# Performance work log

Measured on AMD Instinct MI355X. Metric: run time of the kernel, lower is better.

The kernel has to match this reference:

```python
import jax, jax.numpy as jnp
import numpy as np

N_NODES = 100000
N_GRAPHS = 64


def gcn_layer(x, src, dst, W, b, n):
    # GCNConv: h = x @ W; out_i = sum_j norm_ij * h_j (+ self loop), + bias
    h = x @ W
    deg = jax.ops.segment_sum(jnp.ones(src.shape[0], x.dtype), dst, num_segments=n)
    dinv = jnp.where(deg > 0, jax.lax.rsqrt(deg), 0.0)
    norm = dinv[src] * dinv[dst]                      # [E+N]
    agg = jax.ops.segment_sum(h[src] * norm[:, None], dst, num_segments=n)
    return agg + b


def setup_inputs() -> dict:
    key = jax.random.key(0)
    ks = jax.random.split(key, 12)
    nfeat, nhid, nclass = 128, 64, 10
    E = 1600000
    x = jax.random.normal(ks[0], (N_NODES, nfeat), dtype=jnp.float32)
    edge_index = jax.random.randint(ks[1], (2, E), 0, N_NODES, dtype=jnp.int64)
    batch = jnp.sort(jax.random.randint(ks[2], (N_NODES,), 0, N_GRAPHS, dtype=jnp.int64))
    def w(k, fi, fo):
        return jax.random.normal(k, (fi, fo), dtype=jnp.float32) / np.sqrt(fi)
    return {
        "x": x, "edge_index": edge_index, "batch": batch,
        "W1": w(ks[3], nfeat, nhid), "b1": jnp.zeros((nhid,), jnp.float32),
        "W2": w(ks[4], nhid, nhid), "b2": jnp.zeros((nhid,), jnp.float32),
        "W3": w(ks[5], nhid, nhid), "b3": jnp.zeros((nhid,), jnp.float32),
        "Wl": w(ks[6], nhid, nclass), "bl": jnp.zeros((nclass,), jnp.float32),
    }


def reference(x, edge_index, batch, W1, b1, W2, b2, W3, b3, Wl, bl):
    n = x.shape[0]
    loop = jnp.arange(n, dtype=edge_index.dtype)
    src = jnp.concatenate([edge_index[0], loop])   # self-loops appended
    dst = jnp.concatenate([edge_index[1], loop])
    h = x  # eval mode: dropout is identity; use_bn=False
    for W, b in ((W1, b1), (W2, b2), (W3, b3)):
        h = jax.nn.relu(gcn_layer(h, src, dst, W, b, n))
    # global mean pool per graph
    sums = jax.ops.segment_sum(h, batch, num_segments=N_GRAPHS)
    cnts = jax.ops.segment_sum(jnp.ones((n,), h.dtype), batch, num_segments=N_GRAPHS)
    pooled = sums / jnp.maximum(cnts, 1.0)[:, None]   # [G, nhid]
    logits = pooled @ Wl + bl
    return jax.nn.softmax(logits, axis=1)
```

## Files before the change

kernel.cpp:

```cpp
#include <hip/hip_runtime.h>
#include <math.h>


typedef __attribute__((ext_vector_type(8))) short bf16x8;
typedef __attribute__((ext_vector_type(4))) float f32x4;
typedef __attribute__((ext_vector_type(2))) float f32x2;

__device__ __forceinline__ unsigned short f2bf(float f) {
    unsigned int u = __float_as_uint(f);
    u += 0x7fffu + ((u >> 16) & 1u);
    return (unsigned short)(u >> 16);
}
__device__ __forceinline__ float bf2f(unsigned short u) {
    return __uint_as_float((unsigned int)u << 16);
}
__device__ __forceinline__ float bflo(unsigned int u) {
    return __uint_as_float(u << 16);
}
__device__ __forceinline__ float bfhi(unsigned int u) {
    return __uint_as_float(u & 0xffff0000u);
}


__global__ __launch_bounds__(256) void hist_kernel(const int* __restrict__ dst,
                                                   int* __restrict__ counts,
                                                   int E, int P, int C,
                                                   const float* __restrict__ W1,
                                                   const float* __restrict__ W2,
                                                   const float* __restrict__ W3,
                                                   unsigned short* __restrict__ Wt1,
                                                   unsigned short* __restrict__ Wt2,
                                                   unsigned short* __restrict__ Wt3,
                                                   float* __restrict__ sums, int G) {
    int t = threadIdx.x, b = blockIdx.x;
    if (b >= 256) {
        int xb = b - 256;
        if (xb < 3) {
            const float* W = (xb == 0) ? W1 : ((xb == 1) ? W2 : W3);
            unsigned short* Wt = (xb == 0) ? Wt1 : ((xb == 1) ? Wt2 : Wt3);
            int K = (xb == 0) ? 128 : 64;
            int o = t & 63;
            for (int k = t >> 6; k < K; k += 4)
                Wt[o * K + k] = f2bf(W[k * 64 + o]);
        } else {
            for (int i = t; i < G * 65; i += 256) sums[i] = 0.f;
        }
        return;
    }
    __shared__ int hist[256];
    if (t < P) hist[t] = 0;
    __syncthreads();
    int beg = b * C, end = min(E, beg + C);
    for (int base = beg + t * 8; base < end; base += 2048) {
        if (base + 8 <= end) {
            int4 d0 = *(const int4*)&dst[base];
            int4 d1 = *(const int4*)&dst[base + 4];
            int d[8] = {d0.x, d0.y, d0.z, d0.w, d1.x, d1.y, d1.z, d1.w};
#pragma unroll
            for (int j = 0; j < 8; ++j) atomicAdd(&hist[d[j] >> 9], 1);
        } else {
            for (int e = base; e < end; ++e) atomicAdd(&hist[dst[e] >> 9], 1);
        }
    }
    __syncthreads();
    if (t < P) counts[b * 256 + t] = hist[t];
}

__global__ __launch_bounds__(256) void pscan_kernel(const int* __restrict__ counts,
                                                    int* __restrict__ pbase,
                                                    int P) {
    __shared__ int s[256];
    int t = threadIdx.x;
    int v = 0;
    if (t < P)
        for (int b = 0; b < 256; ++b) v += counts[b * 256 + t];
    s[t] = v;
    __syncthreads();
    for (int off = 1; off < 256; off <<= 1) {
        int u = (t >= off) ? s[t - off] : 0;
        __syncthreads();
        s[t] += u;
        __syncthreads();
    }
    if (t < P) pbase[t] = s[t] - v;
    if (t == 255) pbase[P] = s[255];
}

__global__ __launch_bounds__(256) void offs_kernel(const int* __restrict__ counts,
                                                   const int* __restrict__ pbase,
                                                   int* __restrict__ offs) {
    __shared__ int s[256];
    int t = threadIdx.x, p = blockIdx.x;
    int v = counts[t * 256 + p];
    s[t] = v;
    __syncthreads();
    for (int off = 1; off < 256; off <<= 1) {
        int u = (t >= off) ? s[t - off] : 0;
        __syncthreads();
        s[t] += u;
        __syncthreads();
    }
    offs[p * 256 + t] = pbase[p] + s[t] - v;
}

__global__ __launch_bounds__(256) void bin_kernel(const int* __restrict__ src,
                                                  const int* __restrict__ dst,
                                                  const int* __restrict__ offs,
                                                  unsigned int* __restrict__ binned,
                                                  int E, int P, int C) {
    __shared__ int cur[256];
    int t = threadIdx.x, b = blockIdx.x;
    if (t < P) cur[t] = offs[t * 256 + b];
    __syncthreads();
    int beg = b * C, end = min(E, beg + C);
    for (int base = beg + t * 8; base < end; base += 2048) {
        if (base + 8 <= end) {
            int4 d0 = *(const int4*)&dst[base];
            int4 d1 = *(const int4*)&dst[base + 4];
            int4 s0 = *(const int4*)&src[base];
            int4 s1 = *(const int4*)&src[base + 4];
            int d[8] = {d0.x, d0.y, d0.z, d0.w, d1.x, d1.y, d1.z, d1.w};
            int s[8] = {s0.x, s0.y, s0.z, s0.w, s1.x, s1.y, s1.z, s1.w};
#pragma unroll
            for (int j = 0; j < 8; ++j) {
                int pos = atomicAdd(&cur[d[j] >> 9], 1);
                binned[pos] = ((unsigned int)s[j] << 9) | (unsigned int)(d[j] & 511);
            }
        } else {
            for (int e = base; e < end; ++e) {
                int dd = dst[e], ss = src[e];
                int pos = atomicAdd(&cur[dd >> 9], 1);
                binned[pos] = ((unsigned int)ss << 9) | (unsigned int)(dd & 511);
            }
        }
    }
}

__global__ __launch_bounds__(256) void gemm1_kernel(const float* __restrict__ X,
                                                    const unsigned short* __restrict__ Wt,
                                                    unsigned short* __restrict__ H, int N) {
    constexpr int FIN = 128;
    constexpr int KS = FIN / 32;
    constexpr int LDP = FIN + 8;
    __shared__ unsigned short sX[64 * LDP];
    int t = threadIdx.x;
    int rowBase = blockIdx.x * 64;

    for (int i = t * 4; i < 64 * FIN; i += 1024) {
        int r = i / FIN, c = i - r * FIN;
        int gr = min(rowBase + r, N - 1);
        float4 vv = *(const float4*)(X + (size_t)gr * FIN + c);
        unsigned e0 = __float_as_uint(vv.x) + 0x8000u, e1 = __float_as_uint(vv.y) + 0x8000u;
        unsigned e2 = __float_as_uint(vv.z) + 0x8000u, e3 = __float_as_uint(vv.w) + 0x8000u;
        uint2 pk;
        pk.x = __builtin_amdgcn_perm(e1, e0, 0x07060302);
        pk.y = __builtin_amdgcn_perm(e3, e2, 0x07060302);
        *(uint2*)&sX[r * LDP + c] = pk;
    }
    __syncthreads();

    int wave = t >> 6;
    int lane = t & 63;
    int r = lane & 15, g = lane >> 4;
    int node = rowBase + wave * 16 + r;

    bf16x8 afr[4][KS];
#pragma unroll
    for (int m = 0; m < 4; ++m)
#pragma unroll
        for (int s = 0; s < KS; ++s)
            afr[m][s] = *(const bf16x8*)&Wt[(m * 16 + r) * FIN + s * 32 + g * 8];

    f32x4 acc[4];
#pragma unroll
    for (int m = 0; m < 4; ++m) acc[m] = (f32x4){0.f, 0.f, 0.f, 0.f};

#pragma unroll
    for (int s = 0; s < KS; ++s) {
        bf16x8 bfr = *(const bf16x8*)&sX[(wave * 16 + r) * LDP + s * 32 + g * 8];
#pragma unroll
        for (int m = 0; m < 4; ++m)
            acc[m] = __builtin_amdgcn_mfma_f32_16x16x32_bf16(afr[m][s], bfr, acc[m], 0, 0, 0);
    }

    if (node < N) {
#pragma unroll
        for (int m = 0; m < 4; ++m) {
            ushort4 o;
            o.x = f2bf(acc[m][0]); o.y = f2bf(acc[m][1]);
            o.z = f2bf(acc[m][2]); o.w = f2bf(acc[m][3]);
            *(ushort4*)&H[(size_t)node * 64 + m * 16 + g * 4] = o;
        }
    }
}

__global__ __launch_bounds__(512) void lsort_kernel(const unsigned int* __restrict__ binned,
                                                    const int* __restrict__ pbase,
                                                    float* __restrict__ dinv,
                                                    int* __restrict__ ovfw,
                                                    int* __restrict__ csrw,
                                                    int* __restrict__ ovf, int N) {
    __shared__ int ldeg[512];
    __shared__ int s[512];
    __shared__ int sob[512];
    int t = threadIdx.x, p = blockIdx.x;
    int lo = p << 9;
    ldeg[t] = 0;
    __syncthreads();
    int eBeg = pbase[p], eEnd = pbase[p + 1];
    {
        int j = eBeg + t;
        for (; j + 1536 < eEnd; j += 2048) {
            unsigned int v0 = binned[j], v1 = binned[j + 512];
            unsigned int v2 = binned[j + 1024], v3 = binned[j + 1536];
            atomicAdd(&ldeg[v0 & 511u], 1);
            atomicAdd(&ldeg[v1 & 511u], 1);
            atomicAdd(&ldeg[v2 & 511u], 1);
            atomicAdd(&ldeg[v3 & 511u], 1);
        }
        for (; j < eEnd; j += 512) atomicAdd(&ldeg[binned[j] & 511u], 1);
    }
    __syncthreads();
    int real = ldeg[t];
    int deg1 = real + 1;
    int ovfUsed = (lo + t < N) ? max(deg1 - 24, 0) : 0;
    int gsl = ((ovfUsed + 7) >> 3) << 3;
    s[t] = gsl;
    __syncthreads();
    for (int off = 1; off < 512; off <<= 1) {
        int u = (t >= off) ? s[t - off] : 0;
        __syncthreads();
        s[t] += u;
        __syncthreads();
    }
    int obase = ((eBeg + 7) & ~7) + (p << 12);
    int myOvf = obase + (s[t] - gsl);
    int ow = gsl ? (((myOvf >> 3) << 7) | (gsl >> 3)) : 0;
    if (lo + t < N) {
        dinv[lo + t] = rsqrtf((float)deg1);
        ovfw[lo + t] = ow;
    }
    if (p == 0 && t == 0) dinv[N] = 0.f;
    __syncthreads();
    ldeg[t] = 0;
    sob[t] = myOvf;
    __syncthreads();
    {
        int j = eBeg + t;
        for (; j + 1536 < eEnd; j += 2048) {
            unsigned int v[4] = {binned[j], binned[j + 512],
                                 binned[j + 1024], binned[j + 1536]};
#pragma unroll
            for (int q = 0; q < 4; ++q) {
                int sr = (int)(v[q] >> 9);
                int dl = (int)(v[q] & 511u);
                int i = atomicAdd(&ldeg[dl], 1);
                int ent = sr << 7;
                if (i < 24) csrw[(size_t)(lo + dl) * 24 + i] = ent;
                else        ovf[sob[dl] + i - 24] = ent;
            }
        }
        for (; j < eEnd; j += 512) {
            unsigned int vv = binned[j];
            int sr = (int)(vv >> 9);
            int dl = (int)(vv & 511u);
            int i = atomicAdd(&ldeg[dl], 1);
            int ent = sr << 7;
            if (i < 24) csrw[(size_t)(lo + dl) * 24 + i] = ent;
            else        ovf[sob[dl] + i - 24] = ent;
        }
    }
    __syncthreads();
    if (lo + t < N) {
        int node = lo + t;
        int dcur = ldeg[t];
        int self = node << 7;
        if (dcur < 24) csrw[(size_t)node * 24 + dcur] = self;
        else           ovf[sob[t] + dcur - 24] = self;
        int pad = N << 7;
        for (int k = dcur + 1; k < 24; ++k)
            csrw[(size_t)node * 24 + k] = pad;
        int og = (ow & 127) << 3;
        for (int k = max(dcur + 1 - 24, 0); k < og; ++k)
            ovf[sob[t] + k] = pad;
    }
}

template <int FIN>
__global__ __launch_bounds__(256) void gemm_mfma_kernel(const unsigned short* __restrict__ Xv,
                                                        const unsigned short* __restrict__ Wt,
                                                        unsigned short* __restrict__ H,
                                                        int N) {
    constexpr int KS = FIN / 32;
    constexpr int LDP = FIN + 8;
    __shared__ unsigned short sX[64 * LDP];
    int tid = threadIdx.x;
    int rowBase = blockIdx.x * 64;

    for (int i = tid * 8; i < 64 * FIN; i += 2048) {
        int r = i / FIN, c = i - r * FIN;
        int gr = min(rowBase + r, N - 1);
        uint4 vv = *(const uint4*)(Xv + (size_t)gr * FIN + c);
        *(uint4*)&sX[r * LDP + c] = vv;
    }
    __syncthreads();

    int wave = tid >> 6;
    int lane = tid & 63;
    int r = lane & 15, g = lane >> 4;
    int node = rowBase + wave * 16 + r;

    bf16x8 afr[4][KS];
#pragma unroll
    for (int m = 0; m < 4; ++m)
#pragma unroll
        for (int s = 0; s < KS; ++s)
            afr[m][s] = *(const bf16x8*)&Wt[(m * 16 + r) * FIN + s * 32 + g * 8];

    f32x4 acc[4];
#pragma unroll
    for (int m = 0; m < 4; ++m) acc[m] = (f32x4){0.f, 0.f, 0.f, 0.f};

#pragma unroll
    for (int s = 0; s < KS; ++s) {
        bf16x8 bfr = *(const bf16x8*)&sX[(wave * 16 + r) * LDP + s * 32 + g * 8];
#pragma unroll
        for (int m = 0; m < 4; ++m)
            acc[m] = __builtin_amdgcn_mfma_f32_16x16x32_bf16(afr[m][s], bfr, acc[m], 0, 0, 0);
    }

    if (node < N) {
#pragma unroll
        for (int m = 0; m < 4; ++m) {
            ushort4 o;
            o.x = f2bf(acc[m][0]); o.y = f2bf(acc[m][1]);
            o.z = f2bf(acc[m][2]); o.w = f2bf(acc[m][3]);
            *(ushort4*)&H[(size_t)node * 64 + m * 16 + g * 4] = o;
        }
    }
}

template <int NQ>
__device__ __forceinline__ void gstep(const int* __restrict__ csrw,
                                      const float* __restrict__ dinv,
                                      const char* __restrict__ hb, float di,
                                      int e, int g, int fo, f32x2 acc[4]) {
    int c[NQ];
#pragma unroll
    for (int q = 0; q < NQ; ++q) c[q] = csrw[e + 8 * q + g];
    float w[NQ];
    uint4 u[NQ];
#pragma unroll
    for (int q = 0; q < NQ; ++q) w[q] = dinv[c[q] >> 7];
#pragma unroll
    for (int q = 0; q < NQ; ++q)
        u[q] = *(const uint4*)(hb + c[q] + fo);
#pragma unroll
    for (int q = 0; q < NQ; ++q) {
        float wq = w[q] * di;
        f32x2 w2;
        w2.x = wq; w2.y = wq;
        acc[0] = __builtin_elementwise_fma(w2, (f32x2){bflo(u[q].x), bfhi(u[q].x)}, acc[0]);
        acc[1] = __builtin_elementwise_fma(w2, (f32x2){bflo(u[q].y), bfhi(u[q].y)}, acc[1]);
        acc[2] = __builtin_elementwise_fma(w2, (f32x2){bflo(u[q].z), bfhi(u[q].z)}, acc[2]);
        acc[3] = __builtin_elementwise_fma(w2, (f32x2){bflo(u[q].w), bfhi(u[q].w)}, acc[3]);
    }
}

__global__ __launch_bounds__(256) void gather_kernel(const int* __restrict__ csrw,
                                                     const int* __restrict__ ovf,
                                                     const int* __restrict__ ovfw,
                                                     const float* __restrict__ dinv,
                                                     const unsigned short* __restrict__ h,
                                                     const float* __restrict__ b,
                                                     unsigned short* __restrict__ aggb, int N) {
    int node = (blockIdx.x * 256 + threadIdx.x) >> 6;
    int lane = threadIdx.x & 63;
    if (node >= N) return;
    int g = lane >> 3;
    int f = lane & 7;
    int fo = f * 16;
    float di = dinv[node];

    f32x2 acc[4];
#pragma unroll
    for (int k = 0; k < 4; ++k) acc[k] = (f32x2){0.f, 0.f};

    const char* hb = (const char*)h;
    gstep<3>(csrw, dinv, hb, di, node * 24, g, fo, acc);

    int ow = ovfw[node];
    if (ow) {
        int onb = ow & 127;
        int oe = (ow >> 7) << 3;
        while (onb >= 4) { gstep<4>(ovf, dinv, hb, di, oe, g, fo, acc); oe += 32; onb -= 4; }
        if (onb == 3)      gstep<3>(ovf, dinv, hb, di, oe, g, fo, acc);
        else if (onb == 2) gstep<2>(ovf, dinv, hb, di, oe, g, fo, acc);
        else if (onb == 1) gstep<1>(ovf, dinv, hb, di, oe, g, fo, acc);
    }

    float a[8];
#pragma unroll
    for (int k = 0; k < 4; ++k) { a[2 * k] = acc[k].x; a[2 * k + 1] = acc[k].y; }
#pragma unroll
    for (int k = 0; k < 8; ++k) {
        float v = a[k];
        v += __shfl_xor(v, 8);
        v += __shfl_xor(v, 16);
        v += __shfl_xor(v, 32);
        a[k] = v;
    }
    if (g == 0) {
        float4 bv0 = *(const float4*)&b[f * 8];
        float4 bv1 = *(const float4*)&b[f * 8 + 4];
        float a0 = fmaxf(a[0] + bv0.x, 0.f), a1 = fmaxf(a[1] + bv0.y, 0.f);
        float a2 = fmaxf(a[2] + bv0.z, 0.f), a3 = fmaxf(a[3] + bv0.w, 0.f);
        float a4 = fmaxf(a[4] + bv1.x, 0.f), a5 = fmaxf(a[5] + bv1.y, 0.f);
        float a6 = fmaxf(a[6] + bv1.z, 0.f), a7 = fmaxf(a[7] + bv1.w, 0.f);
        uint4 o;
        o.x = ((unsigned)f2bf(a1) << 16) | f2bf(a0);
        o.y = ((unsigned)f2bf(a3) << 16) | f2bf(a2);
        o.z = ((unsigned)f2bf(a5) << 16) | f2bf(a4);
        o.w = ((unsigned)f2bf(a7) << 16) | f2bf(a6);
        *(uint4*)&aggb[((size_t)node << 6) + f * 8] = o;
    }
}

__global__ __launch_bounds__(256) void pool_kernel(const unsigned short* __restrict__ hb,
                                                   const int* __restrict__ batch,
                                                   float* __restrict__ sums,
                                                   float* __restrict__ cnts, int N) {
    int lane = threadIdx.x & 63;
    int wid = (blockIdx.x * 256 + threadIdx.x) >> 6;
    int base = wid * 32;
    if (base >= N) return;
    int nn = min(N - base, 32);
    int bl = batch[base + min(lane & 31, nn - 1)];

    float v[32];
#pragma unroll
    for (int j = 0; j < 32; ++j) {
        int node = base + min(j, nn - 1);
        v[j] = bf2f(hb[(size_t)node * 64 + lane]);
    }

    int curg = __shfl(bl, 0);
    float acc = 0.f, cnt = 0.f;
#pragma unroll
    for (int j = 0; j < 32; ++j) {
        if (j < nn) {
            int g = __shfl(bl, j);
            if (g != curg) {
                atomicAdd(&sums[curg * 64 + lane], acc);
                if (lane == 0) atomicAdd(&cnts[curg], cnt);
                acc = 0.f; cnt = 0.f; curg = g;
            }
            acc += v[j]; cnt += 1.f;
        }
    }
    atomicAdd(&sums[curg * 64 + lane], acc);
    if (lane == 0) atomicAdd(&cnts[curg], cnt);
}

__global__ void final_kernel(const float* __restrict__ sums, const float* __restrict__ cnts,
                             const float* __restrict__ Wl, const float* __restrict__ bl,
                             float* __restrict__ out, int G) {
    int g = blockIdx.x * blockDim.x + threadIdx.x;
    if (g >= G) return;
    float inv = 1.0f / fmaxf(cnts[g], 1.0f);
    float logits[10];
#pragma unroll
    for (int k = 0; k < 10; ++k) logits[k] = bl[k];
    for (int c = 0; c < 64; ++c) {
        float p = sums[g * 64 + c] * inv;
#pragma unroll
        for (int k = 0; k < 10; ++k) logits[k] = fmaf(p, Wl[c * 10 + k], logits[k]);
    }
    float m = logits[0];
#pragma unroll
    for (int k = 1; k < 10; ++k) m = fmaxf(m, logits[k]);
    float se = 0.f;
#pragma unroll
    for (int k = 0; k < 10; ++k) { logits[k] = expf(logits[k] - m); se += logits[k]; }
    float is = 1.0f / se;
#pragma unroll
    for (int k = 0; k < 10; ++k) out[g * 10 + k] = logits[k] * is;
}

extern "C" void kernel_launch(void* const* d_in, const int* in_sizes, int n_in,
                              void* d_out, int out_size, void* d_ws, size_t ws_size,
                              hipStream_t stream) {
    const float* x    = (const float*)d_in[0];
    const int* edges  = (const int*)d_in[1];
    const int* batch  = (const int*)d_in[2];
    const float* W1   = (const float*)d_in[3];
    const float* b1   = (const float*)d_in[4];
    const float* W2   = (const float*)d_in[5];
    const float* b2   = (const float*)d_in[6];
    const float* W3   = (const float*)d_in[7];
    const float* b3   = (const float*)d_in[8];
    const float* Wl   = (const float*)d_in[9];
    const float* bl   = (const float*)d_in[10];

    const int N = in_sizes[0] / 128;
    const int E = in_sizes[1] / 2;
    const int G = out_size / 10;
    const int* src = edges;
    const int* dst = edges + E;

    float* ws     = (float*)d_ws;
    unsigned short* h = (unsigned short*)ws;
    unsigned short* aggb = (unsigned short*)(ws + (size_t)N * 32);
    unsigned int* binned = (unsigned int*)(ws + (size_t)N * 32);
    size_t o = (size_t)N * 64;
    int*   csrw   = (int*)(ws + o);    o += (size_t)24 * N;
    int*   ovf    = (int*)(ws + o);    o += (size_t)E + 4096 * 256 + 8;
    float* dinv   = ws + o;            o += N + 1;
    int*   ovfw   = (int*)(ws + o);    o += N;
    int*   counts = (int*)(ws + o);    o += 256 * 256;
    int*   offs   = (int*)(ws + o);    o += 256 * 256;
    int*   pbase  = (int*)(ws + o);    o += 257;
    float* sums   = ws + o;            o += (size_t)G * 64;
    float* cnts   = ws + o;            o += G;
    unsigned short* Wt1 = (unsigned short*)(ws + o);
    unsigned short* Wt2 = Wt1 + 64 * 128;
    unsigned short* Wt3 = Wt2 + 64 * 64;

    const int gemmGrid = (N + 63) / 64;
    const int gatherGrid = (N + 3) / 4;
    const int poolGrid = ((N + 31) / 32 + 3) / 4;
    const int P = (N + 511) >> 9;
    const int C = (((E + 255) / 256) + 7) & ~7;

    hist_kernel<<<260, 256, 0, stream>>>(dst, counts, E, P, C,
                                         W1, W2, W3, Wt1, Wt2, Wt3, sums, G);
    pscan_kernel<<<1, 256, 0, stream>>>(counts, pbase, P);
    offs_kernel<<<P, 256, 0, stream>>>(counts, pbase, offs);
    bin_kernel<<<256, 256, 0, stream>>>(src, dst, offs, binned, E, P, C);
    gemm1_kernel<<<gemmGrid, 256, 0, stream>>>(x, Wt1, h, N);
    lsort_kernel<<<P, 512, 0, stream>>>(binned, pbase, dinv, ovfw, csrw, ovf, N);

    gather_kernel<<<gatherGrid, 256, 0, stream>>>(csrw, ovf, ovfw, dinv, h, b1, aggb, N);

    gemm_mfma_kernel<64><<<gemmGrid, 256, 0, stream>>>(aggb, Wt2, h, N);
    gather_kernel<<<gatherGrid, 256, 0, stream>>>(csrw, ovf, ovfw, dinv, h, b2, aggb, N);

    gemm_mfma_kernel<64><<<gemmGrid, 256, 0, stream>>>(aggb, Wt3, h, N);
    gather_kernel<<<gatherGrid, 256, 0, stream>>>(csrw, ovf, ovfw, dinv, h, b3, aggb, N);

    pool_kernel<<<poolGrid, 256, 0, stream>>>(aggb, batch, sums, cnts, N);
    final_kernel<<<1, 64, 0, stream>>>(sums, cnts, Wl, bl, (float*)d_out, G);
}
```

Baseline: 333.9 us.

## Fold prefix-scan kernels into bin and lsort kernels to cut launches

Removes the separate pscan and offs kernels. Each bin block and each lsort block now recomputes the column sums and prefix scan over the 256x256 counts matrix itself. The goal is to drop two kernel launches and the global round trips through pbase and offs. In exchange every block reads the full counts table (256 reads per thread), adding redundant work and memory traffic to both kernels.

```diff
diff --git a/kernel.cpp b/kernel.cpp
--- a/kernel.cpp
+++ b/kernel.cpp
@@ -48,7 +48,7 @@
         return;
     }
     __shared__ int hist[256];
-    if (t < P) hist[t] = 0;
+    hist[t] = 0;
     __syncthreads();
     int beg = b * C, end = min(E, beg + C);
     for (int base = beg + t * 8; base < end; base += 2048) {
@@ -63,18 +63,24 @@
         }
     }
     __syncthreads();
-    if (t < P) counts[b * 256 + t] = hist[t];
-}
-
-__global__ __launch_bounds__(256) void pscan_kernel(const int* __restrict__ counts,
-                                                    int* __restrict__ pbase,
-                                                    int P) {
+    counts[b * 256 + t] = hist[t];
+}
+
+__global__ __launch_bounds__(256) void bin_kernel(const int* __restrict__ src,
+                                                  const int* __restrict__ dst,
+                                                  const int* __restrict__ counts,
+                                                  unsigned int* __restrict__ binned,
+                                                  int E, int C) {
+    __shared__ int cur[256];
     __shared__ int s[256];
-    int t = threadIdx.x;
-    int v = 0;
-    if (t < P)
-        for (int b = 0; b < 256; ++b) v += counts[b * 256 + t];
-    s[t] = v;
+    int t = threadIdx.x, b = blockIdx.x;
+    int colsum = 0, pre = 0;
+    for (int bb = 0; bb < 256; ++bb) {
+        int c = counts[bb * 256 + t];
+        colsum += c;
+        if (bb < b) pre += c;
+    }
+    s[t] = colsum;
     __syncthreads();
     for (int off = 1; off < 256; off <<= 1) {
         int u = (t >= off) ? s[t - off] : 0;
@@ -82,35 +88,7 @@
         s[t] += u;
         __syncthreads();
     }
-    if (t < P) pbase[t] = s[t] - v;
-    if (t == 255) pbase[P] = s[255];
-}
-
-__global__ __launch_bounds__(256) void offs_kernel(const int* __restrict__ counts,
-                                                   const int* __restrict__ pbase,
-                                                   int* __restrict__ offs) {
-    __shared__ int s[256];
-    int t = threadIdx.x, p = blockIdx.x;
-    int v = counts[t * 256 + p];
-    s[t] = v;
-    __syncthreads();
-    for (int off = 1; off < 256; off <<= 1) {
-        int u = (t >= off) ? s[t - off] : 0;
-        __syncthreads();
-        s[t] += u;
-        __syncthreads();
-    }
-    offs[p * 256 + t] = pbase[p] + s[t] - v;
-}
-
-__global__ __launch_bounds__(256) void bin_kernel(const int* __restrict__ src,
-                                                  const int* __restrict__ dst,
-                                                  const int* __restrict__ offs,
-                                                  unsigned int* __restrict__ binned,
-                                                  int E, int P, int C) {
-    __shared__ int cur[256];
-    int t = threadIdx.x, b = blockIdx.x;
-    if (t < P) cur[t] = offs[t * 256 + b];
+    cur[t] = (s[t] - colsum) + pre;
     __syncthreads();
     int beg = b * C, end = min(E, beg + C);
     for (int base = beg + t * 8; base < end; base += 2048) {
@@ -120,11 +98,11 @@
             int4 s0 = *(const int4*)&src[base];
             int4 s1 = *(const int4*)&src[base + 4];
             int d[8] = {d0.x, d0.y, d0.z, d0.w, d1.x, d1.y, d1.z, d1.w};
-            int s[8] = {s0.x, s0.y, s0.z, s0.w, s1.x, s1.y, s1.z, s1.w};
+            int sv[8] = {s0.x, s0.y, s0.z, s0.w, s1.x, s1.y, s1.z, s1.w};
 #pragma unroll
             for (int j = 0; j < 8; ++j) {
                 int pos = atomicAdd(&cur[d[j] >> 9], 1);
-                binned[pos] = ((unsigned int)s[j] << 9) | (unsigned int)(d[j] & 511);
+                binned[pos] = ((unsigned int)sv[j] << 9) | (unsigned int)(d[j] & 511);
             }
         } else {
             for (int e = base; e < end; ++e) {
@@ -195,7 +173,7 @@
 }
 
 __global__ __launch_bounds__(512) void lsort_kernel(const unsigned int* __restrict__ binned,
-                                                    const int* __restrict__ pbase,
+                                                    const int* __restrict__ counts,
                                                     float* __restrict__ dinv,
                                                     int* __restrict__ ovfw,
                                                     int* __restrict__ csrw,
@@ -205,9 +183,22 @@
     __shared__ int sob[512];
     int t = threadIdx.x, p = blockIdx.x;
     int lo = p << 9;
+    int colsum = 0;
+    if (t < 256)
+        for (int bb = 0; bb < 256; ++bb) colsum += counts[bb * 256 + t];
+    s[t] = (t < 256) ? colsum : 0;
+    __syncthreads();
+    for (int off = 1; off < 256; off <<= 1) {
+        int u = (t >= off && t < 256) ? s[t - off] : 0;
+        __syncthreads();
+        if (t < 256) s[t] += u;
+        __syncthreads();
+    }
+    int eBeg = (p > 0) ? s[p - 1] : 0;
+    int eEnd = s[p];
+    __syncthreads();
     ldeg[t] = 0;
     __syncthreads();
-    int eBeg = pbase[p], eEnd = pbase[p + 1];
     {
         int j = eBeg + t;
         for (; j + 1536 < eEnd; j += 2048) {
@@ -518,8 +509,6 @@
     float* dinv   = ws + o;            o += N + 1;
     int*   ovfw   = (int*)(ws + o);    o += N;
     int*   counts = (int*)(ws + o);    o += 256 * 256;
-    int*   offs   = (int*)(ws + o);    o += 256 * 256;
-    int*   pbase  = (int*)(ws + o);    o += 257;
     float* sums   = ws + o;            o += (size_t)G * 64;
     float* cnts   = ws + o;            o += G;
     unsigned short* Wt1 = (unsigned short*)(ws + o);
@@ -534,11 +523,9 @@
 
     hist_kernel<<<260, 256, 0, stream>>>(dst, counts, E, P, C,
                                          W1, W2, W3, Wt1, Wt2, Wt3, sums, G);
-    pscan_kernel<<<1, 256, 0, stream>>>(counts, pbase, P);
-    offs_kernel<<<P, 256, 0, stream>>>(counts, pbase, offs);
-    bin_kernel<<<256, 256, 0, stream>>>(src, dst, offs, binned, E, P, C);
+    bin_kernel<<<256, 256, 0, stream>>>(src, dst, counts, binned, E, C);
     gemm1_kernel<<<gemmGrid, 256, 0, stream>>>(x, Wt1, h, N);
-    lsort_kernel<<<P, 512, 0, stream>>>(binned, pbase, dinv, ovfw, csrw, ovf, N);
+    lsort_kernel<<<P, 512, 0, stream>>>(binned, counts, dinv, ovfw, csrw, ovf, N);
 
     gather_kernel<<<gatherGrid, 256, 0, stream>>>(csrw, ovf, ovfw, dinv, h, b1, aggb, N);
 
```

New measurement: 341.2 us. +2.2%, slower.
